# Kernel tuning notes

Hardware: AMD Instinct MI355X
Metric: run time of the kernel (lower is better)

Reference implementation:

```python
import jax, jax.numpy as jnp
import numpy as np

B, S, C, H = 2, 2048, 1024, 16
D = C // H  # head_size = 64


def setup_inputs() -> dict:
    key = jax.random.key(0)
    ks = jax.random.split(key, 8)
    scale = 1.0 / np.sqrt(C)
    return {
        "src": jax.random.normal(ks[0], (B, S, C), dtype=jnp.float32),
        "Wq": jax.random.normal(ks[1], (C, C), dtype=jnp.float32) * scale,
        "bq": jnp.zeros((C,), dtype=jnp.float32),
        "Wk": jax.random.normal(ks[2], (C, C), dtype=jnp.float32) * scale,
        "bk": jnp.zeros((C,), dtype=jnp.float32),
        "Wv": jax.random.normal(ks[3], (C, C), dtype=jnp.float32) * scale,
        "bv": jnp.zeros((C,), dtype=jnp.float32),
        "rel_k_table": jax.random.normal(ks[4], (2 * S - 1, D), dtype=jnp.float32),
    }


def reference(src, Wq, bq, Wk, bk, Wv, bv, rel_k_table):
    # Linear projections (torch Linear: x @ W.T + b)
    q = src @ Wq.T + bq  # (B,S,C)
    k = src @ Wk.T + bk
    v = src @ Wv.T + bv
    # Faithful to torch .view: raw reshape (B,S,C) -> (B,H,S,D), NOT a transpose split
    q = q.reshape(B, H, S, D)
    k = k.reshape(B, H, S, D)
    v = v.reshape(B, H, S, D)
    # content score: q @ k^T
    content = jnp.einsum("bhsd,bhtd->bhst", q, k)  # (B,H,S,S)
    # relative-position embeddings: (S,S,D)
    pos = jnp.arange(S)
    shifted = pos[None, :] - pos[:, None] + (S - 1)  # (S,S) in [0, 2S-2]
    rel_k = rel_k_table[shifted]  # (S,S,D)
    # q.view(S, B*H, D) @ rel_k.permute(0,2,1): batched over first (query-pos) axis
    q_r = q.reshape(S, B * H, D)
    pos_score = jnp.einsum("sbd,std->sbt", q_r, rel_k)  # (S,BH,S)
    pos_score = jnp.transpose(pos_score, (1, 0, 2)).reshape(B, H, S, S)
    scores = (content + pos_score) / jnp.sqrt(jnp.float32(D))
    attn = jax.nn.softmax(scores, axis=-1)
    out = jnp.einsum("bhst,bhtd->bhsd", attn, v)  # (B,H,S,D)
    out = jnp.transpose(out, (0, 2, 1, 3)).reshape(B, S, C)
    return out
```

## Files before the change

kernel.cpp:

```cpp
#include <hip/hip_runtime.h>
#include <hip/hip_bf16.h>

#define BATCH 2
#define SEQ   2048
#define CH    1024
#define NH    16
#define HD    64
#define BHN   (BATCH*NH)
#define SD    (SEQ*HD)

typedef short v8s __attribute__((ext_vector_type(8)));
typedef short v4s __attribute__((ext_vector_type(4)));
typedef float v4f __attribute__((ext_vector_type(4)));

__device__ __forceinline__ short f2bf(float f) {
    unsigned u = __float_as_uint(f);
    u += 0x7fff + ((u >> 16) & 1);
    return (short)(u >> 16);
}

__device__ __forceinline__ unsigned pk2bf(float a, float b) {
    __hip_bfloat162 h = __float22bfloat162_rn(make_float2(a, b));
    unsigned u;
    __builtin_memcpy(&u, &h, 4);
    return u;
}

__device__ __forceinline__ void gl_lds16(const short* g, short* l) {
    __builtin_amdgcn_global_load_lds(
        (const __attribute__((address_space(1))) void*)g,
        (__attribute__((address_space(3))) void*)l, 16, 0, 0);
}

__global__ __launch_bounds__(256) void cast_all_kernel(
    const float* __restrict__ src, const float* __restrict__ wq,
    const float* __restrict__ wk, const float* __restrict__ wv,
    const float* __restrict__ rel,
    short* __restrict__ xb, short* __restrict__ wqb,
    short* __restrict__ wkb, short* __restrict__ wvb,
    short* __restrict__ relb)
{
    const int z = blockIdx.z;
    const float* s; short* d; int n4;
    switch (z) {
        case 0: s = src; d = xb;   n4 = 1048576; break;
        case 1: s = wq;  d = wqb;  n4 = 262144;  break;
        case 2: s = wk;  d = wkb;  n4 = 262144;  break;
        case 3: s = wv;  d = wvb;  n4 = 262144;  break;
        default: s = rel; d = relb; n4 = 65520;  break;
    }
    for (int i = blockIdx.x * 256 + threadIdx.x; i < n4; i += gridDim.x * 256) {
        float4 v = ((const float4*)s)[i];
        v4s o; o.x = f2bf(v.x); o.y = f2bf(v.y); o.z = f2bf(v.z); o.w = f2bf(v.w);
        ((v4s*)d)[i] = o;
    }
}

__global__ __launch_bounds__(256, 3) void proj_mfma_kernel(
    const short* __restrict__ Xb,
    const short* __restrict__ Wqb, const short* __restrict__ Wkb,
    const short* __restrict__ Wvb,
    const float* __restrict__ bq, const float* __restrict__ bk,
    const float* __restrict__ bv,
    short* __restrict__ qo, short* __restrict__ ko, short* __restrict__ vo)
{
    const int z = blockIdx.z;
    const short* W    = (z == 0) ? Wqb : (z == 1) ? Wkb : Wvb;
    const float* bias = (z == 0) ? bq  : (z == 1) ? bk  : bv;
    short*       out  = (z == 0) ? qo  : (z == 1) ? ko  : vo;
    const float  osc  = (z == 0) ? 0.125f : 1.0f;

    const int m0 = blockIdx.y * 128;
    const int n0 = blockIdx.x * 128;
    const int tid  = threadIdx.x;
    const int w    = tid >> 6;
    const int lane = tid & 63;
    const int l15  = lane & 15;
    const int quad = lane >> 4;
    const int wm = w & 1, wn = w >> 1;

    __shared__ short Al[128 * 32];
    __shared__ short Bl[128 * 32];

    v4f acc[4][4];
#pragma unroll
    for (int i = 0; i < 4; i++)
#pragma unroll
        for (int j = 0; j < 4; j++) acc[i][j] = (v4f)(0.f);

    const int lr = lane >> 2;
    const int lc = (lane & 3) * 8;

    for (int k0 = 0; k0 < 1024; k0 += 32) {
        __syncthreads();
#pragma unroll
        for (int l = 0; l < 2; l++) {
            const int slab = w * 32 + l * 16;
            gl_lds16(Xb + (size_t)(m0 + slab + lr) * 1024 + k0 + lc,
                     &Al[slab * 32]);
            gl_lds16(W + (size_t)(n0 + slab + lr) * 1024 + k0 + lc,
                     &Bl[slab * 32]);
        }
        __syncthreads();
        v8s af[4], bf[4];
#pragma unroll
        for (int mt = 0; mt < 4; mt++)
            af[mt] = *(const v8s*)&Al[(wm * 64 + mt * 16 + l15) * 32 + quad * 8];
#pragma unroll
        for (int nt = 0; nt < 4; nt++)
            bf[nt] = *(const v8s*)&Bl[(wn * 64 + nt * 16 + l15) * 32 + quad * 8];
#pragma unroll
        for (int mt = 0; mt < 4; mt++)
#pragma unroll
            for (int nt = 0; nt < 4; nt++)
                acc[mt][nt] = __builtin_amdgcn_mfma_f32_16x16x32_bf16(
                    af[mt], bf[nt], acc[mt][nt], 0, 0, 0);
    }

    float bv4[4];
#pragma unroll
    for (int nt = 0; nt < 4; nt++)
        bv4[nt] = bias[n0 + wn * 64 + nt * 16 + l15];
#pragma unroll
    for (int mt = 0; mt < 4; mt++)
#pragma unroll
        for (int rg = 0; rg < 4; rg++) {
            const int row = m0 + wm * 64 + mt * 16 + quad * 4 + rg;
#pragma unroll
            for (int nt = 0; nt < 4; nt++)
                out[(size_t)row * 1024 + n0 + wn * 64 + nt * 16 + l15] =
                    f2bf((acc[mt][nt][rg] + bv4[nt]) * osc);
        }
}

__global__ __launch_bounds__(256) void vtrans_kernel(
    const short* __restrict__ v, short* __restrict__ vt)
{
    const int bh = blockIdx.y;
    const int t0 = blockIdx.x * 64;
    const int r = threadIdx.x >> 3;
    const int c = (threadIdx.x & 7) * 8;

    __shared__ short T[64][72];
    *(v8s*)&T[r][c] =
        *(const v8s*)(v + (size_t)bh * SD + (size_t)(t0 + r) * HD + c);
    *(v8s*)&T[r + 32][c] =
        *(const v8s*)(v + (size_t)bh * SD + (size_t)(t0 + r + 32) * HD + c);
    __syncthreads();
    v8s o0, o1;
#pragma unroll
    for (int e = 0; e < 8; e++) {
        const int t = 2 * (threadIdx.x & 7) + (e >> 2) + 16 * (e & 3);
        o0[e] = T[t][r];
        o1[e] = T[t][r + 32];
    }
    *(v8s*)(vt + (size_t)bh * SD + (size_t)r * SEQ + t0 + c) = o0;
    *(v8s*)(vt + (size_t)bh * SD + (size_t)(r + 32) * SEQ + t0 + c) = o1;
}

__global__ __launch_bounds__(512, 4) void attn_mfma_kernel(
    const short* __restrict__ qb, const short* __restrict__ kb,
    const short* __restrict__ vtb, const short* __restrict__ relb,
    float* __restrict__ out)
{
    const int tid  = threadIdx.x;
    const int w    = tid >> 6;
    const int lane = tid & 63;
    const int l15  = lane & 15;
    const int quad = lane >> 4;
    const int bh = blockIdx.y, b = bh >> 4, h = bh & 15;
    const int s0 = blockIdx.x * 128;
    const int i0 = w * 16;

    __shared__ short Kl[2][64][64];
    __shared__ short Vl[2][64][64];
    __shared__ short Rl[256][64];
    __shared__ short Pb[8][16][64];

    v8s qc_f[2], qr_f[2];
#pragma unroll
    for (int kh = 0; kh < 2; kh++) {
        const int row = s0 + i0 + l15;
        qc_f[kh] = *(const v8s*)(qb + (size_t)bh * SD +
                                 (size_t)row * HD + kh * 32 + quad * 8);
        qr_f[kh] = *(const v8s*)(qb + (size_t)row * (BHN * HD) +
                                 bh * HD + kh * 32 + quad * 8);
    }

    int  slv[4];
    bool elo[4];
#pragma unroll
    for (int rg = 0; rg < 4; rg++) {
        const int ii = quad * 4 + rg;
        const int e  = l15 + 15 - ii;
        slv[rg] = quad * 16 + (e & 15);
        elo[rg] = (e < 16);
    }

    const int swz = (quad ^ (l15 & 7)) << 4;
    int kaddr[4];
#pragma unroll
    for (int nt = 0; nt < 4; nt++) kaddr[nt] = ((nt * 16 + l15) << 7) + swz;
    const int paddr = (l15 << 7) + swz;

    const int Bq = 1920 - s0;
    int raddr[5];
#pragma unroll
    for (int jt = 0; jt < 5; jt++) {
        const int lg = 2032 - s0 - i0 + jt * 16 + l15;
        raddr[jt] = ((lg & 255) << 7) + ((quad ^ (lg & 7)) << 4);
    }

    const int strow = tid >> 3;
    const int stc   = ((tid & 7) ^ (strow & 7)) * 8;
    const short* ksrc = kb  + (size_t)bh * SD + (size_t)strow * HD  + stc;
    const short* vsrc = vtb + (size_t)bh * SD + (size_t)strow * SEQ + stc;

#pragma unroll
    for (int g = 0; g < 3; g++) {
        const int lr = Bq + g * 64 + strow;
        const int cr = lr < 4094 ? lr : 4094;
        gl_lds16(relb + (size_t)cr * HD + stc,
                 &Rl[(Bq + g * 64 + w * 8) & 255][0]);
    }
    gl_lds16(ksrc, &Kl[0][w * 8][0]);
    gl_lds16(vsrc, &Vl[0][w * 8][0]);

    v4f o_acc[4];
#pragma unroll
    for (int nt = 0; nt < 4; nt++) o_acc[nt] = (v4f)(0.f);
    float lpart[4] = {0.f, 0.f, 0.f, 0.f};

    int cur = 0;
    for (int t0 = 0; t0 < SEQ; t0 += 64, cur ^= 1) {
        __syncthreads();

        {
            const int tn = (t0 + 64 < SEQ) ? t0 + 64 : 0;
            gl_lds16(ksrc + (size_t)tn * HD, &Kl[cur ^ 1][w * 8][0]);
            gl_lds16(vsrc + tn,              &Vl[cur ^ 1][w * 8][0]);
            const int lr = Bq + t0 + 192 + strow;
            const int cr = lr < 4094 ? lr : 4094;
            gl_lds16(relb + (size_t)cr * HD + stc,
                     &Rl[(Bq + t0 + 192 + w * 8) & 255][0]);
        }

        v4f cacc[4], racc[5];
#pragma unroll
        for (int nt = 0; nt < 4; nt++) cacc[nt] = (v4f)(0.f);
#pragma unroll
        for (int jt = 0; jt < 5; jt++) racc[jt] = (v4f)(0.f);

        const char* kbase = (const char*)Kl + cur * 8192;
        const char* vbase = (const char*)Vl + cur * 8192;
        const char* rbase = (const char*)Rl;

#pragma unroll
        for (int kh = 0; kh < 2; kh++) {
            const int x = kh << 6;
            v8s kf[4], rfj[5];
#pragma unroll
            for (int nt = 0; nt < 4; nt++)
                kf[nt] = *(const v8s*)(kbase + (kaddr[nt] ^ x));
#pragma unroll
            for (int jt = 0; jt < 5; jt++)
                rfj[jt] = *(const v8s*)(rbase + (raddr[jt] ^ x));
            __builtin_amdgcn_s_setprio(1);
#pragma unroll
            for (int nt = 0; nt < 4; nt++)
                cacc[nt] = __builtin_amdgcn_mfma_f32_16x16x32_bf16(
                    qc_f[kh], kf[nt], cacc[nt], 0, 0, 0);
#pragma unroll
            for (int jt = 0; jt < 5; jt++)
                racc[jt] = __builtin_amdgcn_mfma_f32_16x16x32_bf16(
                    qr_f[kh], rfj[jt], racc[jt], 0, 0, 0);
            __builtin_amdgcn_s_setprio(0);
        }
#pragma unroll
        for (int jt = 0; jt < 5; jt++) raddr[jt] = (raddr[jt] + 8192) & 32767;

        unsigned g01[4], g23[4], g4v[4];
#pragma unroll
        for (int rg = 0; rg < 4; rg++) {
            unsigned p01 = pk2bf(racc[0][rg], racc[1][rg]);
            unsigned p23 = pk2bf(racc[2][rg], racc[3][rg]);
            unsigned p4  = (unsigned)(unsigned short)f2bf(racc[4][rg]);
            g01[rg] = (unsigned)__shfl((int)p01, slv[rg]);
            g23[rg] = (unsigned)__shfl((int)p23, slv[rg]);
            g4v[rg] = (unsigned)__shfl((int)p4,  slv[rg]);
        }
#pragma unroll
        for (int rg = 0; rg < 4; rg++) {
            const int ii = quad * 4 + rg;
            const unsigned a01 = g01[rg], a23 = g23[rg], a4 = g4v[rg];
            unsigned pb0 = elo[rg] ? (a01 << 16) : (a01 & 0xffff0000u);
            unsigned pb1 = elo[rg] ? (a01 & 0xffff0000u) : (a23 << 16);
            unsigned pb2 = elo[rg] ? (a23 << 16) : (a23 & 0xffff0000u);
            unsigned pb3 = elo[rg] ? (a23 & 0xffff0000u) : (a4  << 16);
            float p0 = __expf(cacc[0][rg] + __uint_as_float(pb0));
            float p1 = __expf(cacc[1][rg] + __uint_as_float(pb1));
            float p2 = __expf(cacc[2][rg] + __uint_as_float(pb2));
            float p3 = __expf(cacc[3][rg] + __uint_as_float(pb3));
            lpart[rg] += (p0 + p1) + (p2 + p3);
            char* pw = (char*)Pb + w * 2048 + ii * 128 +
                       ((((l15 >> 1) ^ (ii & 7)) << 4) + ((l15 & 1) << 3));
            *(uint2*)pw = make_uint2(pk2bf(p0, p1), pk2bf(p2, p3));
        }

        const char* pbase = (const char*)Pb + w * 2048;
#pragma unroll
        for (int kh = 0; kh < 2; kh++) {
            const int x = kh << 6;
            v8s pa = *(const v8s*)(pbase + (paddr ^ x));
            __builtin_amdgcn_s_setprio(1);
#pragma unroll
            for (int nt = 0; nt < 4; nt++) {
                v8s vf = *(const v8s*)(vbase + (kaddr[nt] ^ x));
                o_acc[nt] = __builtin_amdgcn_mfma_f32_16x16x32_bf16(
                    pa, vf, o_acc[nt], 0, 0, 0);
            }
            __builtin_amdgcn_s_setprio(0);
        }
    }

#pragma unroll
    for (int rg = 0; rg < 4; rg++) {
        float rs = lpart[rg];
#pragma unroll
        for (int off = 1; off < 16; off <<= 1)
            rs += __shfl_xor(rs, off);
        const float inv = 1.f / rs;
        const int row = s0 + i0 + quad * 4 + rg;
        const size_t base = ((size_t)b * SEQ + row) * CH + h * HD;
#pragma unroll
        for (int nt = 0; nt < 4; nt++)
            out[base + nt * 16 + l15] = o_acc[nt][rg] * inv;
    }
}

extern "C" void kernel_launch(void* const* d_in, const int* in_sizes, int n_in,
                              void* d_out, int out_size, void* d_ws, size_t ws_size,
                              hipStream_t stream)
{
    const float* src  = (const float*)d_in[0];
    const float* Wq   = (const float*)d_in[1];
    const float* bq   = (const float*)d_in[2];
    const float* Wk   = (const float*)d_in[3];
    const float* bk   = (const float*)d_in[4];
    const float* Wv   = (const float*)d_in[5];
    const float* bv   = (const float*)d_in[6];
    const float* relk = (const float*)d_in[7];
    float* out = (float*)d_out;

    const size_t nQKV = (size_t)BATCH * SEQ * CH;
    const size_t nW   = (size_t)CH * CH;
    short* qb   = (short*)d_ws;
    short* kb   = qb + nQKV;
    short* vb   = kb + nQKV;
    short* vtb  = vb + nQKV;
    short* xb   = vtb + nQKV;
    short* wqb  = xb + nQKV;
    short* wkb  = wqb + nW;
    short* wvb  = wkb + nW;
    short* relb = wvb + nW;

    cast_all_kernel<<<dim3(512, 1, 5), 256, 0, stream>>>(
        src, Wq, Wk, Wv, relk, xb, wqb, wkb, wvb, relb);

    dim3 gProj(1024 / 128, 4096 / 128, 3);
    proj_mfma_kernel<<<gProj, 256, 0, stream>>>(
        xb, wqb, wkb, wvb, bq, bk, bv, qb, kb, vb);

    dim3 gVt(SEQ / 64, BHN);
    vtrans_kernel<<<gVt, 256, 0, stream>>>(vb, vtb);

    dim3 gAttn(SEQ / 128, BHN);
    attn_mfma_kernel<<<gAttn, 512, 0, stream>>>(qb, kb, vtb, relb, out);
}
```

Before: 238.9 us.

## Fold log2e into Q scale, use raw exp2, byte-perm bias select, reorder grids

Folds log2(e) into the Q projection scale so the attention softmax can use the hardware v_exp_f32 (exp2) directly instead of __expf. The shuffle-and-select used to extract bf16 positional biases becomes ds_bpermute with precomputed byte addresses plus v_perm byte selects. Per-lane LDS addresses and the K/V/rel prefetch pointers are now precomputed and advanced incrementally. The projection and attention grids are transposed so that neighbouring blocks share weights and heads in cache. The aim is fewer VALU instructions in the inner loop and better L2 locality, at the cost of more live registers, which could affect occupancy.

```diff
diff --git a/kernel.cpp b/kernel.cpp
--- a/kernel.cpp
+++ b/kernel.cpp
@@ -25,6 +25,27 @@
     __builtin_memcpy(&u, &h, 4);
     return u;
 }
+
+__device__ __forceinline__ float ex2(float x) {
+    float r; asm("v_exp_f32 %0, %1" : "=v"(r) : "v"(x)); return r;
+}
+
+#if __has_builtin(__builtin_amdgcn_perm)
+#define PERMB(a, b, s) __builtin_amdgcn_perm((a), (b), (s))
+#else
+__device__ __forceinline__ unsigned PERMB(unsigned a, unsigned b, unsigned s) {
+    unsigned r = 0;
+#pragma unroll
+    for (int i = 0; i < 4; i++) {
+        unsigned sb = (s >> (8 * i)) & 0xff, byte;
+        if (sb >= 12) byte = (sb == 12) ? 0u : 0xffu;
+        else if (sb < 4) byte = (b >> (8 * sb)) & 0xff;
+        else byte = (a >> (8 * (sb - 4))) & 0xff;
+        r |= byte << (8 * i);
+    }
+    return r;
+}
+#endif
 
 __device__ __forceinline__ void gl_lds16(const short* g, short* l) {
     __builtin_amdgcn_global_load_lds(
@@ -68,10 +89,10 @@
     const short* W    = (z == 0) ? Wqb : (z == 1) ? Wkb : Wvb;
     const float* bias = (z == 0) ? bq  : (z == 1) ? bk  : bv;
     short*       out  = (z == 0) ? qo  : (z == 1) ? ko  : vo;
-    const float  osc  = (z == 0) ? 0.125f : 1.0f;
-
-    const int m0 = blockIdx.y * 128;
-    const int n0 = blockIdx.x * 128;
+    const float  osc  = (z == 0) ? 0.125f * 1.44269504088896f : 1.0f;
+
+    const int m0 = blockIdx.x * 128;
+    const int n0 = blockIdx.y * 128;
     const int tid  = threadIdx.x;
     const int w    = tid >> 6;
     const int lane = tid & 63;
@@ -168,8 +189,8 @@
     const int lane = tid & 63;
     const int l15  = lane & 15;
     const int quad = lane >> 4;
-    const int bh = blockIdx.y, b = bh >> 4, h = bh & 15;
-    const int s0 = blockIdx.x * 128;
+    const int bh = blockIdx.x, b = bh >> 4, h = bh & 15;
+    const int s0 = blockIdx.y * 128;
     const int i0 = w * 16;
 
     __shared__ short Kl[2][64][64];
@@ -187,21 +208,30 @@
                                  bh * HD + kh * 32 + quad * 8);
     }
 
-    int  slv[4];
-    bool elo[4];
+    int      slv4[4];
+    unsigned selA[4], selB[4], pwoff[4];
 #pragma unroll
     for (int rg = 0; rg < 4; rg++) {
         const int ii = quad * 4 + rg;
         const int e  = l15 + 15 - ii;
-        slv[rg] = quad * 16 + (e & 15);
-        elo[rg] = (e < 16);
+        const bool lo = (e < 16);
+        slv4[rg] = (quad * 16 + (e & 15)) << 2;
+        selA[rg] = lo ? 0x05040c0cu : 0x07060c0cu;
+        selB[rg] = lo ? 0x07060c0cu : 0x01000c0cu;
+        pwoff[rg] = (unsigned)(w * 2048 + ii * 128 +
+                    ((((l15 >> 1) ^ (ii & 7)) << 4) + ((l15 & 1) << 3)));
     }
 
     const int swz = (quad ^ (l15 & 7)) << 4;
-    int kaddr[4];
-#pragma unroll
-    for (int nt = 0; nt < 4; nt++) kaddr[nt] = ((nt * 16 + l15) << 7) + swz;
-    const int paddr = (l15 << 7) + swz;
+    int kaddr[2][4], paddr[2];
+#pragma unroll
+    for (int kh = 0; kh < 2; kh++) {
+        const int x = kh << 6;
+#pragma unroll
+        for (int nt = 0; nt < 4; nt++)
+            kaddr[kh][nt] = (((nt * 16 + l15) << 7) + swz) ^ x;
+        paddr[kh] = ((l15 << 7) + swz) ^ x;
+    }
 
     const int Bq = 1920 - s0;
     int raddr[5];
@@ -218,13 +248,20 @@
 
 #pragma unroll
     for (int g = 0; g < 3; g++) {
-        const int lr = Bq + g * 64 + strow;
-        const int cr = lr < 4094 ? lr : 4094;
+        const int lr2 = Bq + g * 64 + strow;
+        const int cr = lr2 < 4094 ? lr2 : 4094;
         gl_lds16(relb + (size_t)cr * HD + stc,
                  &Rl[(Bq + g * 64 + w * 8) & 255][0]);
     }
     gl_lds16(ksrc, &Kl[0][w * 8][0]);
     gl_lds16(vsrc, &Vl[0][w * 8][0]);
+
+    const short* kp = ksrc + 4096;
+    const short* vp = vsrc + 64;
+    const char*  relbp = (const char*)relb + stc * 2;
+    unsigned roff = (unsigned)(Bq + 192 + strow) * 128;
+    const unsigned ROMAX = 4094u * 128;
+    unsigned rlds = (unsigned)((Bq + 192 + w * 8) & 255) << 7;
 
     v4f o_acc[4];
 #pragma unroll
@@ -236,14 +273,16 @@
         __syncthreads();
 
         {
-            const int tn = (t0 + 64 < SEQ) ? t0 + 64 : 0;
-            gl_lds16(ksrc + (size_t)tn * HD, &Kl[cur ^ 1][w * 8][0]);
-            gl_lds16(vsrc + tn,              &Vl[cur ^ 1][w * 8][0]);
-            const int lr = Bq + t0 + 192 + strow;
-            const int cr = lr < 4094 ? lr : 4094;
-            gl_lds16(relb + (size_t)cr * HD + stc,
-                     &Rl[(Bq + t0 + 192 + w * 8) & 255][0]);
-        }
+            short* kd = &Kl[0][w * 8][0];
+            short* vd = &Vl[0][w * 8][0];
+            const int nb = (cur ^ 1) << 12;
+            gl_lds16(kp, kd + nb);
+            gl_lds16(vp, vd + nb);
+            unsigned rc = roff < ROMAX ? roff : ROMAX;
+            gl_lds16((const short*)(relbp + rc), (short*)((char*)Rl + rlds));
+        }
+        kp += 4096; vp += 64; roff += 8192;
+        rlds = (rlds + 8192) & 32767;
 
         v4f cacc[4], racc[5];
 #pragma unroll
@@ -257,14 +296,13 @@
 
 #pragma unroll
         for (int kh = 0; kh < 2; kh++) {
-            const int x = kh << 6;
             v8s kf[4], rfj[5];
 #pragma unroll
             for (int nt = 0; nt < 4; nt++)
-                kf[nt] = *(const v8s*)(kbase + (kaddr[nt] ^ x));
+                kf[nt] = *(const v8s*)(kbase + kaddr[kh][nt]);
 #pragma unroll
             for (int jt = 0; jt < 5; jt++)
-                rfj[jt] = *(const v8s*)(rbase + (raddr[jt] ^ x));
+                rfj[jt] = *(const v8s*)(rbase + (raddr[jt] ^ (kh << 6)));
             __builtin_amdgcn_s_setprio(1);
 #pragma unroll
             for (int nt = 0; nt < 4; nt++)
@@ -284,38 +322,35 @@
         for (int rg = 0; rg < 4; rg++) {
             unsigned p01 = pk2bf(racc[0][rg], racc[1][rg]);
             unsigned p23 = pk2bf(racc[2][rg], racc[3][rg]);
-            unsigned p4  = (unsigned)(unsigned short)f2bf(racc[4][rg]);
-            g01[rg] = (unsigned)__shfl((int)p01, slv[rg]);
-            g23[rg] = (unsigned)__shfl((int)p23, slv[rg]);
-            g4v[rg] = (unsigned)__shfl((int)p4,  slv[rg]);
+            unsigned p4  = pk2bf(racc[4][rg], racc[4][rg]);
+            g01[rg] = (unsigned)__builtin_amdgcn_ds_bpermute(slv4[rg], (int)p01);
+            g23[rg] = (unsigned)__builtin_amdgcn_ds_bpermute(slv4[rg], (int)p23);
+            g4v[rg] = (unsigned)__builtin_amdgcn_ds_bpermute(slv4[rg], (int)p4);
         }
 #pragma unroll
         for (int rg = 0; rg < 4; rg++) {
-            const int ii = quad * 4 + rg;
             const unsigned a01 = g01[rg], a23 = g23[rg], a4 = g4v[rg];
-            unsigned pb0 = elo[rg] ? (a01 << 16) : (a01 & 0xffff0000u);
-            unsigned pb1 = elo[rg] ? (a01 & 0xffff0000u) : (a23 << 16);
-            unsigned pb2 = elo[rg] ? (a23 << 16) : (a23 & 0xffff0000u);
-            unsigned pb3 = elo[rg] ? (a23 & 0xffff0000u) : (a4  << 16);
-            float p0 = __expf(cacc[0][rg] + __uint_as_float(pb0));
-            float p1 = __expf(cacc[1][rg] + __uint_as_float(pb1));
-            float p2 = __expf(cacc[2][rg] + __uint_as_float(pb2));
-            float p3 = __expf(cacc[3][rg] + __uint_as_float(pb3));
+            unsigned pb0 = PERMB(a01, a01, selA[rg]);
+            unsigned pb1 = PERMB(a01, a23, selB[rg]);
+            unsigned pb2 = PERMB(a23, a23, selA[rg]);
+            unsigned pb3 = PERMB(a23, a4,  selB[rg]);
+            float p0 = ex2(cacc[0][rg] + __uint_as_float(pb0));
+            float p1 = ex2(cacc[1][rg] + __uint_as_float(pb1));
+            float p2 = ex2(cacc[2][rg] + __uint_as_float(pb2));
+            float p3 = ex2(cacc[3][rg] + __uint_as_float(pb3));
             lpart[rg] += (p0 + p1) + (p2 + p3);
-            char* pw = (char*)Pb + w * 2048 + ii * 128 +
-                       ((((l15 >> 1) ^ (ii & 7)) << 4) + ((l15 & 1) << 3));
-            *(uint2*)pw = make_uint2(pk2bf(p0, p1), pk2bf(p2, p3));
+            *(uint2*)((char*)Pb + pwoff[rg]) =
+                make_uint2(pk2bf(p0, p1), pk2bf(p2, p3));
         }
 
         const char* pbase = (const char*)Pb + w * 2048;
 #pragma unroll
         for (int kh = 0; kh < 2; kh++) {
-            const int x = kh << 6;
-            v8s pa = *(const v8s*)(pbase + (paddr ^ x));
+            v8s pa = *(const v8s*)(pbase + paddr[kh]);
             __builtin_amdgcn_s_setprio(1);
 #pragma unroll
             for (int nt = 0; nt < 4; nt++) {
-                v8s vf = *(const v8s*)(vbase + (kaddr[nt] ^ x));
+                v8s vf = *(const v8s*)(vbase + kaddr[kh][nt]);
                 o_acc[nt] = __builtin_amdgcn_mfma_f32_16x16x32_bf16(
                     pa, vf, o_acc[nt], 0, 0, 0);
             }
@@ -367,13 +402,13 @@
     cast_all_kernel<<<dim3(512, 1, 5), 256, 0, stream>>>(
         src, Wq, Wk, Wv, relk, xb, wqb, wkb, wvb, relb);
 
-    dim3 gProj(1024 / 128, 4096 / 128, 3);
+    dim3 gProj(4096 / 128, 1024 / 128, 3);
     proj_mfma_kernel<<<gProj, 256, 0, stream>>>(
         xb, wqb, wkb, wvb, bq, bk, bv, qb, kb, vb);
 
     dim3 gVt(SEQ / 64, BHN);
     vtrans_kernel<<<gVt, 256, 0, stream>>>(vb, vtb);
 
-    dim3 gAttn(SEQ / 128, BHN);
+    dim3 gAttn(BHN, SEQ / 128);
     attn_mfma_kernel<<<gAttn, 512, 0, stream>>>(qb, kb, vtb, relb, out);
 }
```

New measurement: 238.2 us. About the same (-0.3%).
